# Optimization experiments

Measured on AMD Instinct MI355X. Metric: run time of the kernel, lower is better.

The kernel has to match this reference:

```python
import jax, jax.numpy as jnp
import numpy as np

B, CDD, L, T, H, NH = 16, 10, 64, 128, 768, 12
DH = H // NH          # head dim = 64
S = CDD * L + T       # full sequence = 768 (640 candidate tokens + 128 terms)


def setup_inputs() -> dict:
    key = jax.random.key(0)
    ks = jax.random.split(key, 7)
    w = 0.02
    return {
        "hidden_states": jax.random.normal(ks[0], (B, S, H), jnp.float32),
        "Wq": jax.random.normal(ks[1], (H, H), jnp.float32) * w,
        "bq": jax.random.normal(ks[2], (H,), jnp.float32) * w,
        "Wk": jax.random.normal(ks[3], (H, H), jnp.float32) * w,
        "bk": jax.random.normal(ks[4], (H,), jnp.float32) * w,
        "Wv": jax.random.normal(ks[5], (H, H), jnp.float32) * w,
        "bv": jax.random.normal(ks[6], (H,), jnp.float32) * w,
    }


def _one_pass_mask(dtype):
    # block-diagonal over candidates + dense global columns for terms
    block = jnp.kron(jnp.eye(CDD, dtype=dtype), jnp.ones((L, L), dtype=dtype))  # [CDD*L, CDD*L]
    return jnp.concatenate([block, jnp.ones((CDD * L, T), dtype=dtype)], axis=-1)  # [CDD*L, S]


def reference(hidden_states, Wq, bq, Wk, bk, Wv, bv):
    def split_heads(x):  # [B, s, H] -> [B, NH, s, DH]
        return x.reshape(B, -1, NH, DH).transpose(0, 2, 1, 3)

    attn_field = hidden_states[:, :-T]                     # [B, CDD*L, H] queries only
    q = split_heads(attn_field @ Wq.T + bq)                # [B, NH, CDD*L, DH]
    k = split_heads(hidden_states @ Wk.T + bk)             # [B, NH, S, DH]
    v = split_heads(hidden_states @ Wv.T + bv)             # [B, NH, S, DH]

    mask = _one_pass_mask(q.dtype)                         # [CDD*L, S]
    scale = 1.0 / np.sqrt(DH).astype(np.float32)
    # NOTE: original multiplies scores by the mask (masked entries become 0, not -inf)
    scores = jnp.einsum('bhqd,bhkd->bhqk', q, k) * scale * mask
    probs = jax.nn.softmax(scores, axis=-1)                # [B, NH, CDD*L, S]

    ctx = jnp.einsum('bhqk,bhkd->bhqd', probs, v)          # [B, NH, CDD*L, DH]
    ctx = jnp.concatenate([ctx, v[:, :, -T:]], axis=2)     # append term values untouched
    return ctx.transpose(0, 2, 1, 3).reshape(B, S, H)
```

## Files before the change

### kernel.cpp

```cpp
#include <hip/hip_runtime.h>

constexpr int Bb  = 16;
constexpr int CDD = 10;
constexpr int Lc  = 64;
constexpr int T   = 128;
constexpr int H   = 768;
constexpr int NH  = 12;
constexpr int DH  = 64;
constexpr int S   = 768;
constexpr int SQ  = 640;
constexpr int MROWS = Bb * S;

typedef __attribute__((ext_vector_type(8))) short bf16x8;
typedef __attribute__((ext_vector_type(4))) short bf16x4;
typedef __attribute__((ext_vector_type(4))) float f32x4;

__device__ inline unsigned short f2bf(float f) {
  unsigned u = __float_as_uint(f);
  u += 0x7fff + ((u >> 16) & 1);
  return (unsigned short)(u >> 16);
}
__device__ inline float bf2f(unsigned short h) {
  return __uint_as_float(((unsigned)h) << 16);
}

__device__ inline void gld_lds16(const void* g, void* l) {
  __builtin_amdgcn_global_load_lds(
      (const __attribute__((address_space(1))) void*)g,
      (__attribute__((address_space(3))) void*)l, 16, 0, 0);
}

__device__ inline bf16x8 ld_b64x2(const unsigned short* p) {
  union { bf16x8 v; bf16x4 h[2]; } u;
  u.h[0] = *(const bf16x4*)p;
  u.h[1] = *(const bf16x4*)(p + 4);
  return u.v;
}

constexpr int NX4 = MROWS * H / 4;
constexpr int NW4 = H * H / 4;
__global__ void convert_all(const float* __restrict__ X,
                            const float* __restrict__ Wq,
                            const float* __restrict__ Wk,
                            const float* __restrict__ Wv,
                            unsigned short* __restrict__ Xb,
                            unsigned short* __restrict__ Wb) {
  int i = blockIdx.x * blockDim.x + threadIdx.x;
  const int stride = gridDim.x * blockDim.x;
  const int total = NX4 + 3 * NW4;
  for (; i < total; i += stride) {
    const float* src;
    unsigned short* dst;
    int off;
    if (i < NX4) {
      src = X; dst = Xb; off = i;
    } else {
      int k = i - NX4;
      int w = k / NW4;
      off = k - w * NW4;
      src = (w == 0) ? Wq : (w == 1) ? Wk : Wv;
      dst = Wb + (size_t)w * H * H;
    }
    float4 v = ((const float4*)src)[off];
    ushort4 o;
    o.x = f2bf(v.x); o.y = f2bf(v.y); o.z = f2bf(v.z); o.w = f2bf(v.w);
    ((ushort4*)dst)[off] = o;
  }
}

__launch_bounds__(256, 4)
__global__ void qkv_gemm(const unsigned short* __restrict__ Xb,
                         const unsigned short* __restrict__ Wb,
                         const float* __restrict__ bq, const float* __restrict__ bk,
                         const float* __restrict__ bv,
                         unsigned short* __restrict__ Qb, unsigned short* __restrict__ Kb,
                         unsigned short* __restrict__ Vb,
                         float* __restrict__ out) {
  const int z = blockIdx.z;
  const unsigned short* W = Wb + (size_t)z * H * H;
  const float* bias = (z == 0) ? bq : (z == 1) ? bk : bv;
  unsigned short* Y = (z == 0) ? Qb : (z == 1) ? Kb : Vb;

  const int i0 = blockIdx.x * 128;
  const int j0 = blockIdx.y * 128;
  const int tid = threadIdx.x;
  const int wave = tid >> 6, lane = tid & 63;
  const int wr = wave >> 1, wc = wave & 1;
  const int col = lane & 15, quad = lane >> 4;

  __shared__ unsigned short As[128 * 32];
  __shared__ unsigned short Bs[128 * 32];

  f32x4 acc[4][4];
#pragma unroll
  for (int i = 0; i < 4; i++)
#pragma unroll
    for (int j = 0; j < 4; j++) acc[i][j] = (f32x4){0.f, 0.f, 0.f, 0.f};

  const int rowA0 = tid >> 2, csA0 = tid & 3;
  const int rowA1 = (tid + 256) >> 2, csA1 = tid & 3;
  const int gcA0 = csA0 ^ ((rowA0 >> 1) & 3);
  const int gcA1 = csA1 ^ ((rowA1 >> 1) & 3);

  for (int kt = 0; kt < 24; kt++) {
    const int k0 = kt * 32;
    gld_lds16(Xb + (size_t)(i0 + rowA0) * H + k0 + gcA0 * 8, &As[tid * 8]);
    gld_lds16(Xb + (size_t)(i0 + rowA1) * H + k0 + gcA1 * 8, &As[(tid + 256) * 8]);
    gld_lds16(W  + (size_t)(j0 + rowA0) * H + k0 + gcA0 * 8, &Bs[tid * 8]);
    gld_lds16(W  + (size_t)(j0 + rowA1) * H + k0 + gcA1 * 8, &Bs[(tid + 256) * 8]);
    __builtin_amdgcn_s_waitcnt(0);
    __syncthreads();

    bf16x8 a[4], b[4];
#pragma unroll
    for (int mt = 0; mt < 4; mt++) {
      int r = wr * 64 + mt * 16 + col;
      a[mt] = *(const bf16x8*)&As[r * 32 + ((quad ^ ((r >> 1) & 3)) * 8)];
    }
#pragma unroll
    for (int nt = 0; nt < 4; nt++) {
      int r = wc * 64 + nt * 16 + col;
      b[nt] = *(const bf16x8*)&Bs[r * 32 + ((quad ^ ((r >> 1) & 3)) * 8)];
    }
#pragma unroll
    for (int mt = 0; mt < 4; mt++)
#pragma unroll
      for (int nt = 0; nt < 4; nt++)
        acc[mt][nt] = __builtin_amdgcn_mfma_f32_16x16x32_bf16(a[mt], b[nt], acc[mt][nt], 0, 0, 0);
    __syncthreads();
  }

#pragma unroll
  for (int mt = 0; mt < 4; mt++) {
#pragma unroll
    for (int nt = 0; nt < 4; nt++) {
      const int j = j0 + wc * 64 + nt * 16 + col;
      const float bj = bias[j];
#pragma unroll
      for (int r = 0; r < 4; r++) {
        const int i = i0 + wr * 64 + mt * 16 + quad * 4 + r;
        const float v = acc[mt][nt][r] + bj;
        Y[(size_t)i * H + j] = f2bf(v);
        if (z == 2) {
          int s = i - (i / S) * S;
          if (s >= SQ) out[(size_t)i * H + j] = v;
        }
      }
    }
  }
}

__global__ void vtot_partial(const unsigned short* __restrict__ Vb,
                             float* __restrict__ part) {
  const int b = blockIdx.x;
  const int j = blockIdx.y * 256 + threadIdx.x;
  const int rs = blockIdx.z;
  const unsigned short* p = Vb + (size_t)(b * S + rs * 96) * H + j;
  float s = 0.f;
#pragma unroll 8
  for (int r = 0; r < 96; r++) s += bf2f(p[(size_t)r * H]);
  part[(size_t)(b * 8 + rs) * H + j] = s;
}

__launch_bounds__(256, 2)
__global__ void attn_kernel(const unsigned short* __restrict__ Qb,
                            const unsigned short* __restrict__ Kb,
                            const unsigned short* __restrict__ Vb,
                            const float* __restrict__ part,
                            float* __restrict__ out) {
  const int bid = blockIdx.x;
  const int c = bid % CDD;
  const int h = (bid / CDD) % NH;
  const int b = bid / (CDD * NH);
  const int tid = threadIdx.x;
  const int wave = tid >> 6, lane = tid & 63;
  const int col = lane & 15, quad = lane >> 4;

  __shared__ __align__(16) char smem[59136];
  unsigned short* Qs = (unsigned short*)smem;
  unsigned short* Ks = (unsigned short*)(smem + 8192);
  unsigned short* Ps = (unsigned short*)smem;
  unsigned short* Vt = (unsigned short*)(smem + 32768);
  float* red   = (float*)(smem + 57856);
  float* vcorr = (float*)(smem + 58880);

  const size_t rowQ0 = (size_t)(b * S + c * 64) * H + h * DH;

  {
    int s0 = tid, s1 = tid + 256;
    int r0 = s0 >> 3, g0 = (s0 & 7) ^ (r0 & 7);
    int r1 = s1 >> 3, g1 = (s1 & 7) ^ (r1 & 7);
    gld_lds16(Qb + rowQ0 + (size_t)r0 * H + g0 * 8, &Qs[s0 * 8]);
    gld_lds16(Qb + rowQ0 + (size_t)r1 * H + g1 * 8, &Qs[s1 * 8]);
  }
#pragma unroll
  for (int j = 0; j < 6; j++) {
    int s = tid + 256 * j;
    int key = s >> 3;
    int gkey = (key < 64) ? (c * 64 + key) : (576 + key);
    int gc = (s & 7) ^ (key & 7);
    gld_lds16(Kb + (size_t)(b * S + gkey) * H + h * DH + gc * 8, &Ks[s * 8]);
  }
#pragma unroll
  for (int j = 0; j < 6; j++) {
    int s = tid + 256 * j;
    int key = s >> 3;
    int f0 = (s & 7) * 8;
    int gkey = (key < 64) ? (c * 64 + key) : (576 + key);
    union { int4 i4; unsigned short u[8]; } uv;
    uv.i4 = *(const int4*)(Vb + (size_t)(b * S + gkey) * H + h * DH + f0);
#pragma unroll
    for (int i = 0; i < 8; i++) Vt[(f0 + i) * 196 + key] = uv.u[i];
  }
  __builtin_amdgcn_s_waitcnt(0);
  __syncthreads();

  {
    int d = tid & 63, p = tid >> 6;
    float sum = 0.f;
    for (int k = p * 48; k < p * 48 + 48; k++) sum += bf2f(Vt[d * 196 + k]);
    red[tid] = sum;
  }
  __syncthreads();
  if (tid < 64) {
    float tot = 0.f;
#pragma unroll
    for (int rs = 0; rs < 8; rs++) tot += part[(size_t)(b * 8 + rs) * H + h * DH + tid];
    vcorr[tid] = tot - (red[tid] + red[64 + tid] + red[128 + tid] + red[192 + tid]);
  }

  f32x4 sc[12];
#pragma unroll
  for (int n = 0; n < 12; n++) sc[n] = (f32x4){0.f, 0.f, 0.f, 0.f};
  {
    const int rq = wave * 16 + col;
    bf16x8 a0 = *(const bf16x8*)&Qs[rq * 64 + ((quad ^ (rq & 7)) * 8)];
    bf16x8 a1 = *(const bf16x8*)&Qs[rq * 64 + (((4 + quad) ^ (rq & 7)) * 8)];
#pragma unroll
    for (int n = 0; n < 12; n++) {
      const int rk = n * 16 + col;
      bf16x8 b0 = *(const bf16x8*)&Ks[rk * 64 + ((quad ^ (rk & 7)) * 8)];
      bf16x8 b1 = *(const bf16x8*)&Ks[rk * 64 + (((4 + quad) ^ (rk & 7)) * 8)];
      sc[n] = __builtin_amdgcn_mfma_f32_16x16x32_bf16(a0, b0, sc[n], 0, 0, 0);
      sc[n] = __builtin_amdgcn_mfma_f32_16x16x32_bf16(a1, b1, sc[n], 0, 0, 0);
    }
  }

  float em[4], zin[4];
  {
    const float scale = 0.125f;
#pragma unroll
    for (int r = 0; r < 4; r++) {
      float mx = sc[0][r];
#pragma unroll
      for (int n = 1; n < 12; n++) mx = fmaxf(mx, sc[n][r]);
#pragma unroll
      for (int msk = 1; msk <= 8; msk <<= 1) mx = fmaxf(mx, __shfl_xor(mx, msk, 64));
      const float mrow = fmaxf(mx * scale, 0.f);
      float rs = 0.f;
#pragma unroll
      for (int n = 0; n < 12; n++) {
        float p = __expf(sc[n][r] * scale - mrow);
        sc[n][r] = p;
        rs += p;
      }
#pragma unroll
      for (int msk = 1; msk <= 8; msk <<= 1) rs += __shfl_xor(rs, msk, 64);
      const float e = __expf(-mrow);
      em[r] = e;
      zin[r] = 1.f / (rs + 576.f * e);
    }
  }
  __syncthreads();

#pragma unroll
  for (int n = 0; n < 12; n++)
#pragma unroll
    for (int r = 0; r < 4; r++)
      Ps[(wave * 16 + quad * 4 + r) * 196 + n * 16 + col] = f2bf(sc[n][r]);
  __syncthreads();

  f32x4 o[4];
#pragma unroll
  for (int n2 = 0; n2 < 4; n2++) o[n2] = (f32x4){0.f, 0.f, 0.f, 0.f};
#pragma unroll
  for (int ks = 0; ks < 6; ks++) {
    bf16x8 a = ld_b64x2(&Ps[(wave * 16 + col) * 196 + ks * 32 + quad * 8]);
#pragma unroll
    for (int n2 = 0; n2 < 4; n2++) {
      bf16x8 bvv = ld_b64x2(&Vt[(n2 * 16 + col) * 196 + ks * 32 + quad * 8]);
      o[n2] = __builtin_amdgcn_mfma_f32_16x16x32_bf16(a, bvv, o[n2], 0, 0, 0);
    }
  }

#pragma unroll
  for (int n2 = 0; n2 < 4; n2++) {
    const int d = n2 * 16 + col;
    const float vc = vcorr[d];
#pragma unroll
    for (int r = 0; r < 4; r++) {
      const int m = wave * 16 + quad * 4 + r;
      const float val = (o[n2][r] + em[r] * vc) * zin[r];
      out[(size_t)(b * S + c * 64 + m) * H + h * DH + d] = val;
    }
  }
}

extern "C" void kernel_launch(void* const* d_in, const int* in_sizes, int n_in,
                              void* d_out, int out_size, void* d_ws, size_t ws_size,
                              hipStream_t stream) {
  const float* X  = (const float*)d_in[0];
  const float* Wq = (const float*)d_in[1];
  const float* bq = (const float*)d_in[2];
  const float* Wk = (const float*)d_in[3];
  const float* bk = (const float*)d_in[4];
  const float* Wv = (const float*)d_in[5];
  const float* bv = (const float*)d_in[6];
  float* out = (float*)d_out;

  char* ws = (char*)d_ws;
  unsigned short* Xb   = (unsigned short*)ws;
  unsigned short* Wb   = (unsigned short*)(ws + 18874368);
  unsigned short* Qb   = (unsigned short*)(ws + 22413312);
  unsigned short* Kb   = (unsigned short*)(ws + 41287680);
  unsigned short* Vb   = (unsigned short*)(ws + 60162048);
  float*          part = (float*)(ws + 79036416);

  convert_all<<<2048, 256, 0, stream>>>(X, Wq, Wk, Wv, Xb, Wb);
  qkv_gemm<<<dim3(96, 6, 3), 256, 0, stream>>>(Xb, Wb, bq, bk, bv, Qb, Kb, Vb, out);
  vtot_partial<<<dim3(16, 3, 8), 256, 0, stream>>>(Vb, part);
  attn_kernel<<<1920, 256, 0, stream>>>(Qb, Kb, Vb, part, out);
}
```

Measured before the change: 193.4 us.

## Fuse V column sums into QKV GEMM, skip unused Q tiles, load Q/K directly

The separate vtot_partial kernel is removed. Per-batch V column sums are now accumulated in the QKV GEMM epilogue with wave shuffles and atomicAdd, into a buffer zeroed by a memset. The GEMM also skips Q blocks covering the term rows, whose queries are never used. The attention kernel loads Q and K fragments straight from global memory into registers instead of staging them in LDS. This shrinks shared memory and lets launch bounds rise to 3 blocks per SM, at the cost of redundant global K loads across waves and nondeterministic atomic summation order.

```diff
diff --git a/kernel.cpp b/kernel.cpp
--- a/kernel.cpp
+++ b/kernel.cpp
@@ -75,8 +75,10 @@
                          const float* __restrict__ bv,
                          unsigned short* __restrict__ Qb, unsigned short* __restrict__ Kb,
                          unsigned short* __restrict__ Vb,
+                         float* __restrict__ part,
                          float* __restrict__ out) {
   const int z = blockIdx.z;
+  if (z == 0 && (blockIdx.x % 6) == 5) return;
   const unsigned short* W = Wb + (size_t)z * H * H;
   const float* bias = (z == 0) ? bq : (z == 1) ? bk : bv;
   unsigned short* Y = (z == 0) ? Qb : (z == 1) ? Kb : Vb;
@@ -130,6 +132,7 @@
     __syncthreads();
   }
 
+  float colsum[4] = {0.f, 0.f, 0.f, 0.f};
 #pragma unroll
   for (int mt = 0; mt < 4; mt++) {
 #pragma unroll
@@ -142,27 +145,29 @@
         const float v = acc[mt][nt][r] + bj;
         Y[(size_t)i * H + j] = f2bf(v);
         if (z == 2) {
+          colsum[nt] += v;
           int s = i - (i / S) * S;
           if (s >= SQ) out[(size_t)i * H + j] = v;
         }
       }
     }
   }
-}
-
-__global__ void vtot_partial(const unsigned short* __restrict__ Vb,
-                             float* __restrict__ part) {
-  const int b = blockIdx.x;
-  const int j = blockIdx.y * 256 + threadIdx.x;
-  const int rs = blockIdx.z;
-  const unsigned short* p = Vb + (size_t)(b * S + rs * 96) * H + j;
-  float s = 0.f;
-#pragma unroll 8
-  for (int r = 0; r < 96; r++) s += bf2f(p[(size_t)r * H]);
-  part[(size_t)(b * 8 + rs) * H + j] = s;
-}
-
-__launch_bounds__(256, 2)
+  if (z == 2) {
+    const int b = blockIdx.x / 6;
+#pragma unroll
+    for (int nt = 0; nt < 4; nt++) {
+      float s = colsum[nt];
+      s += __shfl_xor(s, 16, 64);
+      s += __shfl_xor(s, 32, 64);
+      if (quad == 0) {
+        const int j = j0 + wc * 64 + nt * 16 + col;
+        atomicAdd(&part[b * H + j], s);
+      }
+    }
+  }
+}
+
+__launch_bounds__(256, 3)
 __global__ void attn_kernel(const unsigned short* __restrict__ Qb,
                             const unsigned short* __restrict__ Kb,
                             const unsigned short* __restrict__ Vb,
@@ -176,31 +181,11 @@
   const int wave = tid >> 6, lane = tid & 63;
   const int col = lane & 15, quad = lane >> 4;
 
-  __shared__ __align__(16) char smem[59136];
-  unsigned short* Qs = (unsigned short*)smem;
-  unsigned short* Ks = (unsigned short*)(smem + 8192);
-  unsigned short* Ps = (unsigned short*)smem;
-  unsigned short* Vt = (unsigned short*)(smem + 32768);
-  float* red   = (float*)(smem + 57856);
-  float* vcorr = (float*)(smem + 58880);
-
-  const size_t rowQ0 = (size_t)(b * S + c * 64) * H + h * DH;
-
-  {
-    int s0 = tid, s1 = tid + 256;
-    int r0 = s0 >> 3, g0 = (s0 & 7) ^ (r0 & 7);
-    int r1 = s1 >> 3, g1 = (s1 & 7) ^ (r1 & 7);
-    gld_lds16(Qb + rowQ0 + (size_t)r0 * H + g0 * 8, &Qs[s0 * 8]);
-    gld_lds16(Qb + rowQ0 + (size_t)r1 * H + g1 * 8, &Qs[s1 * 8]);
-  }
-#pragma unroll
-  for (int j = 0; j < 6; j++) {
-    int s = tid + 256 * j;
-    int key = s >> 3;
-    int gkey = (key < 64) ? (c * 64 + key) : (576 + key);
-    int gc = (s & 7) ^ (key & 7);
-    gld_lds16(Kb + (size_t)(b * S + gkey) * H + h * DH + gc * 8, &Ks[s * 8]);
-  }
+  __shared__ __align__(16) char smem[51200];
+  unsigned short* Vt = (unsigned short*)smem;
+  unsigned short* Ps = (unsigned short*)(smem + 25088);
+  float* red = (float*)(smem + 50176);
+
 #pragma unroll
   for (int j = 0; j < 6; j++) {
     int s = tid + 256 * j;
@@ -212,7 +197,53 @@
 #pragma unroll
     for (int i = 0; i < 8; i++) Vt[(f0 + i) * 196 + key] = uv.u[i];
   }
-  __builtin_amdgcn_s_waitcnt(0);
+
+  f32x4 sc[12];
+#pragma unroll
+  for (int n = 0; n < 12; n++) sc[n] = (f32x4){0.f, 0.f, 0.f, 0.f};
+  {
+    const unsigned short* qrow =
+        Qb + (size_t)(b * S + c * 64 + wave * 16 + col) * H + h * DH;
+    bf16x8 a0 = *(const bf16x8*)(qrow + quad * 8);
+    bf16x8 a1 = *(const bf16x8*)(qrow + 32 + quad * 8);
+#pragma unroll
+    for (int n = 0; n < 12; n++) {
+      const int rk = n * 16 + col;
+      const int gkey = (rk < 64) ? (c * 64 + rk) : (576 + rk);
+      const unsigned short* krow = Kb + (size_t)(b * S + gkey) * H + h * DH;
+      bf16x8 b0 = *(const bf16x8*)(krow + quad * 8);
+      bf16x8 b1 = *(const bf16x8*)(krow + 32 + quad * 8);
+      sc[n] = __builtin_amdgcn_mfma_f32_16x16x32_bf16(a0, b0, sc[n], 0, 0, 0);
+      sc[n] = __builtin_amdgcn_mfma_f32_16x16x32_bf16(a1, b1, sc[n], 0, 0, 0);
+    }
+  }
+
+  float em[4], zin[4];
+  {
+    const float scale = 0.125f;
+#pragma unroll
+    for (int r = 0; r < 4; r++) {
+      float mx = sc[0][r];
+#pragma unroll
+      for (int n = 1; n < 12; n++) mx = fmaxf(mx, sc[n][r]);
+#pragma unroll
+      for (int msk = 1; msk <= 8; msk <<= 1) mx = fmaxf(mx, __shfl_xor(mx, msk, 64));
+      const float mrow = fmaxf(mx * scale, 0.f);
+      float rs = 0.f;
+#pragma unroll
+      for (int n = 0; n < 12; n++) {
+        float p = __expf(sc[n][r] * scale - mrow);
+        sc[n][r] = p;
+        rs += p;
+      }
+#pragma unroll
+      for (int msk = 1; msk <= 8; msk <<= 1) rs += __shfl_xor(rs, msk, 64);
+      const float e = __expf(-mrow);
+      em[r] = e;
+      zin[r] = 1.f / (rs + 576.f * e);
+    }
+  }
+
   __syncthreads();
 
   {
@@ -221,58 +252,6 @@
     for (int k = p * 48; k < p * 48 + 48; k++) sum += bf2f(Vt[d * 196 + k]);
     red[tid] = sum;
   }
-  __syncthreads();
-  if (tid < 64) {
-    float tot = 0.f;
-#pragma unroll
-    for (int rs = 0; rs < 8; rs++) tot += part[(size_t)(b * 8 + rs) * H + h * DH + tid];
-    vcorr[tid] = tot - (red[tid] + red[64 + tid] + red[128 + tid] + red[192 + tid]);
-  }
-
-  f32x4 sc[12];
-#pragma unroll
-  for (int n = 0; n < 12; n++) sc[n] = (f32x4){0.f, 0.f, 0.f, 0.f};
-  {
-    const int rq = wave * 16 + col;
-    bf16x8 a0 = *(const bf16x8*)&Qs[rq * 64 + ((quad ^ (rq & 7)) * 8)];
-    bf16x8 a1 = *(const bf16x8*)&Qs[rq * 64 + (((4 + quad) ^ (rq & 7)) * 8)];
-#pragma unroll
-    for (int n = 0; n < 12; n++) {
-      const int rk = n * 16 + col;
-      bf16x8 b0 = *(const bf16x8*)&Ks[rk * 64 + ((quad ^ (rk & 7)) * 8)];
-      bf16x8 b1 = *(const bf16x8*)&Ks[rk * 64 + (((4 + quad) ^ (rk & 7)) * 8)];
-      sc[n] = __builtin_amdgcn_mfma_f32_16x16x32_bf16(a0, b0, sc[n], 0, 0, 0);
-      sc[n] = __builtin_amdgcn_mfma_f32_16x16x32_bf16(a1, b1, sc[n], 0, 0, 0);
-    }
-  }
-
-  float em[4], zin[4];
-  {
-    const float scale = 0.125f;
-#pragma unroll
-    for (int r = 0; r < 4; r++) {
-      float mx = sc[0][r];
-#pragma unroll
-      for (int n = 1; n < 12; n++) mx = fmaxf(mx, sc[n][r]);
-#pragma unroll
-      for (int msk = 1; msk <= 8; msk <<= 1) mx = fmaxf(mx, __shfl_xor(mx, msk, 64));
-      const float mrow = fmaxf(mx * scale, 0.f);
-      float rs = 0.f;
-#pragma unroll
-      for (int n = 0; n < 12; n++) {
-        float p = __expf(sc[n][r] * scale - mrow);
-        sc[n][r] = p;
-        rs += p;
-      }
-#pragma unroll
-      for (int msk = 1; msk <= 8; msk <<= 1) rs += __shfl_xor(rs, msk, 64);
-      const float e = __expf(-mrow);
-      em[r] = e;
-      zin[r] = 1.f / (rs + 576.f * e);
-    }
-  }
-  __syncthreads();
-
 #pragma unroll
   for (int n = 0; n < 12; n++)
 #pragma unroll
@@ -296,7 +275,8 @@
 #pragma unroll
   for (int n2 = 0; n2 < 4; n2++) {
     const int d = n2 * 16 + col;
-    const float vc = vcorr[d];
+    const float vc = part[b * H + h * DH + d] -
+                     (red[d] + red[64 + d] + red[128 + d] + red[192 + d]);
 #pragma unroll
     for (int r = 0; r < 4; r++) {
       const int m = wave * 16 + quad * 4 + r;
@@ -326,8 +306,8 @@
   unsigned short* Vb   = (unsigned short*)(ws + 60162048);
   float*          part = (float*)(ws + 79036416);
 
+  hipMemsetAsync(part, 0, Bb * H * sizeof(float), stream);
   convert_all<<<2048, 256, 0, stream>>>(X, Wq, Wk, Wv, Xb, Wb);
-  qkv_gemm<<<dim3(96, 6, 3), 256, 0, stream>>>(Xb, Wb, bq, bk, bv, Qb, Kb, Vb, out);
-  vtot_partial<<<dim3(16, 3, 8), 256, 0, stream>>>(Vb, part);
+  qkv_gemm<<<dim3(96, 6, 3), 256, 0, stream>>>(Xb, Wb, bq, bk, bv, Qb, Kb, Vb, part, out);
   attn_kernel<<<1920, 256, 0, stream>>>(Qb, Kb, Vb, part, out);
 }
```

New measurement: 189.7 us. No clear change (-1.9%).
